# Kernel optimization log

Hardware: AMD Instinct MI355X
Metric: run time of the kernel (lower is better)

## Reference

```python
import jax, jax.numpy as jnp
import numpy as np

B, L, NSTATE = 8192, 256, 9


def setup_inputs() -> dict:
    key = jax.random.key(0)
    k1, k2, k3, k4 = jax.random.split(key, 4)
    inputs = jax.random.normal(k1, (B, L, NSTATE), dtype=jnp.float32)
    path = jax.random.randint(k2, (B, L), 0, NSTATE, dtype=jnp.int32)
    # learned CRF params (init'd to zeros in the module; use small random for a
    # non-degenerate reference)
    tran = jax.random.normal(k3, (NSTATE, NSTATE), dtype=jnp.float32) * 0.1
    init = jax.random.normal(k4, (NSTATE,), dtype=jnp.float32) * 0.1
    return {"inputs": inputs, "path": path, "tran": tran, "init": init}


def reference(inputs, path, tran, init):
    # inputs: [B, L, S], path: [B, L], tran: [S, S], init: [S]
    # bio=False -> mask and imask are all zeros (no-op additions).
    # --- gold path score ---
    emit = jnp.take_along_axis(inputs, path[..., None], axis=-1)[..., 0]  # [B, L]
    tran_sc = tran[path[..., :-1], path[..., 1:]]                         # [B, L-1]
    path_scores = emit.sum(-1) + init[path[..., 0]] + tran_sc.sum(-1)     # [B]

    # --- partition function via log-semiring forward recurrence ---
    alpha0 = init + inputs[..., 0, :]                                     # [B, S]

    def step(alpha, x_t):
        # alpha: [B, S] (prev state), x_t: [B, S] (emission at t)
        nxt = alpha[..., :, None] + tran + x_t[..., None, :]              # [B, S, S]
        return jax.nn.logsumexp(nxt, axis=-2), None

    xs = jnp.moveaxis(inputs[..., 1:, :], -2, 0)                          # [L-1, B, S]
    alpha, _ = jax.lax.scan(step, alpha0, xs)
    scores = jax.nn.logsumexp(alpha, axis=-1)                             # [B]
    return scores - path_scores
```

## Files before the change

### kernel.cpp

```cpp
#include <hip/hip_runtime.h>


#define B_N 8192
#define L_N 256
#define SEQ_STRIDE 2304
#define HALF 128
#define SPB 6
#define XW 54
#define XSTRIDE 55
#define NBLK 22
#define PLS 129
#define SPW 16
#define NDIR_BLOCKS (B_N / SPW)

#define LOG2E 1.44269504088896340736f
#define LN2f  0.69314718055994530942f

#define QP1 57
#define QP2 78
#define QP3 147
#define QROT(src, CTRL) \
  __int_as_float(__builtin_amdgcn_mov_dpp(__float_as_int(src), CTRL, 0xf, 0xf, 0))

#define WAITV0 asm volatile("s_waitcnt vmcnt(0)" ::: "memory")

__device__ __forceinline__ void gl_lds4(const void* g, void* l) {
  __builtin_amdgcn_global_load_lds(
      (const __attribute__((address_space(1))) void*)g,
      (__attribute__((address_space(3))) void*)l, 4, 0, 0);
}

__device__ __forceinline__ float fexp(float x) {
  return __builtin_amdgcn_exp2f(x * LOG2E);
}

#define FWD_STEP_BODY(KK, DO_RESC)                                          \
  do {                                                                      \
    float g[4][3];                                                          \
    _Pragma("unroll") for (int k = 0; k < 3; ++k) {                         \
      g[0][k] = o[k];                                                       \
      g[1][k] = QROT(o[k], QP1);                                            \
      g[2][k] = QROT(o[k], QP2);                                            \
      g[3][k] = QROT(o[k], QP3);                                            \
    }                                                                       \
    if (DO_RESC) {                                                          \
      float m = g[0][0];                                                    \
      _Pragma("unroll") for (int r = 0; r < 4; ++r)                         \
        _Pragma("unroll") for (int k = 0; k < 3; ++k)                       \
          m = fmaxf(m, g[r][k]);                                            \
      const int ex = (int)((__float_as_uint(m) >> 23) & 0xffu) - 126;       \
      ce += ex;                                                             \
      const float sc = __uint_as_float((unsigned)(127 - ex) << 23);         \
      _Pragma("unroll") for (int r = 0; r < 4; ++r)                         \
        _Pragma("unroll") for (int k = 0; k < 3; ++k)                       \
          g[r][k] *= sc;                                                    \
    }                                                                       \
    float out3[3];                                                          \
    _Pragma("unroll") for (int i = 0; i < 3; ++i) {                         \
      float a = Erot[0][0][i] * g[0][0];                                    \
      _Pragma("unroll") for (int r = 0; r < 4; ++r)                         \
        _Pragma("unroll") for (int k = 0; k < 3; ++k)                       \
          if (r + k > 0) a = fmaf(Erot[r][k][i], g[r][k], a);               \
      out3[i] = a;                                                          \
    }                                                                       \
    _Pragma("unroll") for (int i = 0; i < 3; ++i)                           \
      o[i] = out3[i] * e[(KK) * 3 + i];                                     \
  } while (0)

#define BWD_STEP_BODY(KK, DO_RESC)                                          \
  do {                                                                      \
    const int tt_ = 5 - (KK);                                               \
    float wv[3];                                                            \
    _Pragma("unroll") for (int k = 0; k < 3; ++k)                           \
      wv[k] = e[tt_ * 3 + k] * o[k];                                        \
    float g[4][3];                                                          \
    _Pragma("unroll") for (int k = 0; k < 3; ++k) {                         \
      g[0][k] = wv[k];                                                      \
      g[1][k] = QROT(wv[k], QP1);                                           \
      g[2][k] = QROT(wv[k], QP2);                                           \
      g[3][k] = QROT(wv[k], QP3);                                           \
    }                                                                       \
    if (DO_RESC) {                                                          \
      float m = g[0][0];                                                    \
      _Pragma("unroll") for (int r = 0; r < 4; ++r)                         \
        _Pragma("unroll") for (int k = 0; k < 3; ++k)                       \
          m = fmaxf(m, g[r][k]);                                            \
      const int ex = (int)((__float_as_uint(m) >> 23) & 0xffu) - 126;       \
      ce += ex;                                                             \
      const float sc = __uint_as_float((unsigned)(127 - ex) << 23);         \
      _Pragma("unroll") for (int r = 0; r < 4; ++r)                         \
        _Pragma("unroll") for (int k = 0; k < 3; ++k)                       \
          g[r][k] *= sc;                                                    \
    }                                                                       \
    float out3[3];                                                          \
    _Pragma("unroll") for (int i = 0; i < 3; ++i) {                         \
      float a = Erot[0][0][i] * g[0][0];                                    \
      _Pragma("unroll") for (int r = 0; r < 4; ++r)                         \
        _Pragma("unroll") for (int k = 0; k < 3; ++k)                       \
          if (r + k > 0) a = fmaf(Erot[r][k][i], g[r][k], a);               \
      out3[i] = a;                                                          \
    }                                                                       \
    _Pragma("unroll") for (int i = 0; i < 3; ++i) o[i] = out3[i];           \
  } while (0)

#define PREFETCH_WIN(NB)                                                    \
  if (lane < XW) {                                                          \
    const int fb = fwd ? (NB) * XW : (SEQ_STRIDE - XW * ((NB) + 1));        \
    float* dst = &lx[(NB) & 1][0];                                          \
    _Pragma("unroll") for (int r = 0; r < SPW; ++r)                         \
      gl_lds4(xg + (size_t)(seq0 + r) * SEQ_STRIDE + fb + lane,             \
              dst + r * XSTRIDE);                                           \
  }

#define EBATCH(T0, T1)                                                      \
  _Pragma("unroll") for (int tt = (T0); tt <= (T1); ++tt)                   \
    _Pragma("unroll") for (int k = 0; k < 3; ++k)                           \
      e[tt * 3 + k] = fexp(lxq[tt * 9 + myoff + k]);

#define EMTR_FWD(N)                                                         \
  _Pragma("unroll") for (int kk = 0; kk < (N); ++kk) {                      \
    em[kk] = lxq[kk * 9 + pc6[kk]];                                         \
    const int pp = kk ? pc6[kk - 1] : pcur;                                 \
    tr[kk] = ltran[pp * 9 + pc6[kk]];                                       \
  }

#define EMTR_BWD(N)                                                         \
  _Pragma("unroll") for (int kk = 0; kk < (N); ++kk) {                      \
    const int pc = kk ? pc6[kk - 1] : pcur;                                 \
    em[kk] = lxq[(5 - kk) * 9 + pc];                                        \
    tr[kk] = ltran[pc6[kk] * 9 + pc];                                       \
  }

#define PREREAD_PN(TBN)                                                     \
  if (fwd) {                                                                \
    _Pragma("unroll") for (int kk = 0; kk < SPB; ++kk) {                    \
      int t = (TBN) + kk; if (t > HALF - 1) t = HALF - 1;                   \
      pn6[kk] = plr[t];                                                     \
    }                                                                       \
  } else {                                                                  \
    _Pragma("unroll") for (int kk = 0; kk < SPB; ++kk) {                    \
      int idx = 127 - (TBN) - kk; if (idx < 0) idx = 0;                     \
      pn6[kk] = plr[idx];                                                   \
    }                                                                       \
  }

__global__ __launch_bounds__(64, 1) void crf_half(
    const float* __restrict__ xg, const int* __restrict__ path,
    const float* __restrict__ tran, const float* __restrict__ initv,
    float* __restrict__ ws)
{
  __shared__ float lx[2][SPW * XSTRIDE];
  __shared__ int   pl[SPW * PLS];
  __shared__ int   pl255[SPW];
  __shared__ float ltran[81];

  const int lane = threadIdx.x;
  const int c = lane & 3;
  const int q = lane >> 2;
  const bool fwd = (int)blockIdx.x < NDIR_BLOCKS;
  const int seq0 = (fwd ? blockIdx.x : blockIdx.x - NDIR_BLOCKS) * SPW;

  for (int i = lane; i < 81; i += 64) ltran[i] = tran[i];

  {
    const int t0 = fwd ? 0 : 127;
#pragma unroll
    for (int r = 0; r < SPW; ++r) {
      const int* g = path + (size_t)(seq0 + r) * L_N + t0 + lane;
      gl_lds4(g,      &pl[r * PLS]);
      gl_lds4(g + 64, &pl[r * PLS + 64]);
    }
  }
  if (!fwd && lane < SPW)
    pl255[lane] = path[(size_t)(seq0 + lane) * L_N + 255];
  if (lane < XW) {
    const int fb = fwd ? 0 : (SEQ_STRIDE - XW);
#pragma unroll
    for (int r = 0; r < SPW; ++r)
      gl_lds4(xg + (size_t)(seq0 + r) * SEQ_STRIDE + fb + lane,
              &lx[0][r * XSTRIDE]);
  }

  float Erot[4][3][3];
#pragma unroll
  for (int r = 0; r < 4; ++r)
#pragma unroll
    for (int k = 0; k < 3; ++k)
#pragma unroll
      for (int i = 0; i < 3; ++i) {
        const int ig = 3 * c + i;
        const int jg = 3 * ((c + r) & 3) + k;
        float v = 0.f;
        if (ig < 9 && jg < 9)
          v = fexp(fwd ? tran[jg * 9 + ig] : tran[ig * 9 + jg]);
        Erot[r][k][i] = v;
      }

  float iv[3];
#pragma unroll
  for (int k = 0; k < 3; ++k) {
    iv[k] = (fwd && c < 3) ? initv[3 * c + k] : 0.f;
    asm volatile("" :: "v"(iv[k]));
  }

  float o[3];
  float emit = 0.f, trn = 0.f;
  int ce = 0, pcur = 0;
  if (!fwd) {
#pragma unroll
    for (int k = 0; k < 3; ++k) o[k] = (c < 3) ? 1.f : 0.f;
  }

  const int myoff = (c == 3) ? 0 : 3 * c;
  const int* plr = &pl[q * PLS];

  WAITV0;
  if (!fwd) pcur = pl255[q];

  int pc6[SPB];
  if (fwd) {
#pragma unroll
    for (int kk = 0; kk < SPB; ++kk) pc6[kk] = plr[kk];
  } else {
#pragma unroll
    for (int kk = 0; kk < SPB; ++kk) pc6[kk] = plr[127 - kk];
  }

  {
    PREFETCH_WIN(1)
    const float* lxq = &lx[0][q * XSTRIDE];
    float e[SPB * 3];
    EBATCH(0, 5)
    float em[SPB], tr[SPB];
    int pn6[SPB];
    if (fwd) { EMTR_FWD(6) } else { EMTR_BWD(6) }
    PREREAD_PN(SPB)
    if (fwd) {
#pragma unroll
      for (int k = 0; k < 3; ++k)
        o[k] = (c < 3) ? fexp(iv[k] + lxq[myoff + k]) : 0.f;
      FWD_STEP_BODY(1, false);
      FWD_STEP_BODY(2, false);
      FWD_STEP_BODY(3, false);
      FWD_STEP_BODY(4, false);
      FWD_STEP_BODY(5, false);
#pragma unroll
      for (int kk = 0; kk < 6; ++kk) emit += em[kk];
#pragma unroll
      for (int kk = 1; kk < 6; ++kk) trn += tr[kk];
    } else {
      BWD_STEP_BODY(0, false);
      BWD_STEP_BODY(1, false);
      BWD_STEP_BODY(2, false);
      BWD_STEP_BODY(3, false);
      BWD_STEP_BODY(4, false);
      BWD_STEP_BODY(5, false);
#pragma unroll
      for (int kk = 0; kk < 6; ++kk) { emit += em[kk]; trn += tr[kk]; }
    }
    pcur = pc6[SPB - 1];
#pragma unroll
    for (int kk = 0; kk < SPB; ++kk) pc6[kk] = pn6[kk];
  }

#pragma unroll 1
  for (int b = 1; b <= 20; ++b) {
    const int tb = b * SPB;
    WAITV0;
    PREFETCH_WIN(b + 1)
    const float* lxq = &lx[b & 1][q * XSTRIDE];
    float e[SPB * 3];
    EBATCH(0, 5)
    float em[SPB], tr[SPB];
    int pn6[SPB];
    if (fwd) { EMTR_FWD(6) } else { EMTR_BWD(6) }
    PREREAD_PN(tb + SPB)
    if (fwd) {
      FWD_STEP_BODY(0, true);
      FWD_STEP_BODY(1, false);
      FWD_STEP_BODY(2, false);
      FWD_STEP_BODY(3, false);
      FWD_STEP_BODY(4, false);
      FWD_STEP_BODY(5, false);
    } else {
      BWD_STEP_BODY(0, true);
      BWD_STEP_BODY(1, false);
      BWD_STEP_BODY(2, false);
      BWD_STEP_BODY(3, false);
      BWD_STEP_BODY(4, false);
      BWD_STEP_BODY(5, false);
    }
#pragma unroll
    for (int kk = 0; kk < 6; ++kk) { emit += em[kk]; trn += tr[kk]; }
    pcur = pc6[SPB - 1];
#pragma unroll
    for (int kk = 0; kk < SPB; ++kk) pc6[kk] = pn6[kk];
  }

  {
    WAITV0;
    const float* lxq = &lx[1][q * XSTRIDE];
    float e[SPB * 3];
    float em[SPB], tr[SPB];
    if (fwd) {
      EBATCH(0, 1)
      EMTR_FWD(2)
      FWD_STEP_BODY(0, true);
      FWD_STEP_BODY(1, false);
    } else {
      EBATCH(4, 5)
      EMTR_BWD(2)
      BWD_STEP_BODY(0, true);
      BWD_STEP_BODY(1, false);
    }
#pragma unroll
    for (int kk = 0; kk < 2; ++kk) { emit += em[kk]; trn += tr[kk]; }
  }

  const int sq = seq0 + q;
  float* wp = ws + sq;
  if (fwd) {
    if (c < 3) {
#pragma unroll
      for (int k = 0; k < 3; ++k) wp[(3 * c + k) * B_N] = o[k];
    } else {
      wp[9 * B_N] = (float)ce;
      wp[10 * B_N] = emit + trn + initv[plr[0]];
    }
  } else {
    if (c < 3) {
#pragma unroll
      for (int k = 0; k < 3; ++k) wp[(11 + 3 * c + k) * B_N] = o[k];
    } else {
      wp[20 * B_N] = (float)ce;
      wp[21 * B_N] = emit + trn;
    }
  }
}

__global__ __launch_bounds__(256) void crf_combine(
    const float* __restrict__ ws, float* __restrict__ out)
{
  const int s = blockIdx.x * 256 + threadIdx.x;
  float dot = 0.f;
#pragma unroll
  for (int i = 0; i < 9; ++i)
    dot = fmaf(ws[i * B_N + s], ws[(11 + i) * B_N + s], dot);
  const float score =
      (__builtin_amdgcn_logf(dot) + ws[9 * B_N + s] + ws[20 * B_N + s]) * LN2f;
  out[s] = score - (ws[10 * B_N + s] + ws[21 * B_N + s]);
}

extern "C" void kernel_launch(void* const* d_in, const int* in_sizes, int n_in,
                              void* d_out, int out_size, void* d_ws, size_t ws_size,
                              hipStream_t stream) {
  (void)in_sizes; (void)n_in; (void)out_size; (void)ws_size;
  const float* xg    = (const float*)d_in[0];
  const int*   path  = (const int*)d_in[1];
  const float* tran  = (const float*)d_in[2];
  const float* initv = (const float*)d_in[3];
  float* ws  = (float*)d_ws;
  float* out = (float*)d_out;

  crf_half<<<2 * NDIR_BLOCKS, 64, 0, stream>>>(xg, path, tran, initv, ws);
  crf_combine<<<B_N / 256, 256, 0, stream>>>(ws, out);
}
```

Before: 126.5 us.

## Triple-buffer emission windows and software-pipeline exp/gather one block ahead

```diff
diff --git a/kernel.cpp b/kernel.cpp
--- a/kernel.cpp
+++ b/kernel.cpp
@@ -8,7 +8,6 @@
 #define SPB 6
 #define XW 54
 #define XSTRIDE 55
-#define NBLK 22
 #define PLS 129
 #define SPW 16
 #define NDIR_BLOCKS (B_N / SPW)
@@ -22,7 +21,8 @@
 #define QROT(src, CTRL) \
   __int_as_float(__builtin_amdgcn_mov_dpp(__float_as_int(src), CTRL, 0xf, 0xf, 0))
 
-#define WAITV0 asm volatile("s_waitcnt vmcnt(0)" ::: "memory")
+#define WAITV0  asm volatile("s_waitcnt vmcnt(0)" ::: "memory")
+#define WAITV16 asm volatile("s_waitcnt vmcnt(16)" ::: "memory")
 
 __device__ __forceinline__ void gl_lds4(const void* g, void* l) {
   __builtin_amdgcn_global_load_lds(
@@ -34,7 +34,7 @@
   return __builtin_amdgcn_exp2f(x * LOG2E);
 }
 
-#define FWD_STEP_BODY(KK, DO_RESC)                                          \
+#define FWD_STEP_BODY(KK, EA, DO_RESC)                                      \
   do {                                                                      \
     float g[4][3];                                                          \
     _Pragma("unroll") for (int k = 0; k < 3; ++k) {                         \
@@ -64,15 +64,15 @@
       out3[i] = a;                                                          \
     }                                                                       \
     _Pragma("unroll") for (int i = 0; i < 3; ++i)                           \
-      o[i] = out3[i] * e[(KK) * 3 + i];                                     \
+      o[i] = out3[i] * EA[(KK) * 3 + i];                                    \
   } while (0)
 
-#define BWD_STEP_BODY(KK, DO_RESC)                                          \
+#define BWD_STEP_BODY(KK, EA, DO_RESC)                                      \
   do {                                                                      \
     const int tt_ = 5 - (KK);                                               \
     float wv[3];                                                            \
     _Pragma("unroll") for (int k = 0; k < 3; ++k)                           \
-      wv[k] = e[tt_ * 3 + k] * o[k];                                        \
+      wv[k] = EA[tt_ * 3 + k] * o[k];                                       \
     float g[4][3];                                                          \
     _Pragma("unroll") for (int k = 0; k < 3; ++k) {                         \
       g[0][k] = wv[k];                                                      \
@@ -106,42 +106,48 @@
 #define PREFETCH_WIN(NB)                                                    \
   if (lane < XW) {                                                          \
     const int fb = fwd ? (NB) * XW : (SEQ_STRIDE - XW * ((NB) + 1));        \
-    float* dst = &lx[(NB) & 1][0];                                          \
+    float* dst = &lx[(NB) % 3][0];                                          \
     _Pragma("unroll") for (int r = 0; r < SPW; ++r)                         \
       gl_lds4(xg + (size_t)(seq0 + r) * SEQ_STRIDE + fb + lane,             \
               dst + r * XSTRIDE);                                           \
   }
 
-#define EBATCH(T0, T1)                                                      \
-  _Pragma("unroll") for (int tt = (T0); tt <= (T1); ++tt)                   \
+#define EBATCH_TO(EA, LXQ)                                                  \
+  _Pragma("unroll") for (int tt = 0; tt < 6; ++tt)                          \
     _Pragma("unroll") for (int k = 0; k < 3; ++k)                           \
-      e[tt * 3 + k] = fexp(lxq[tt * 9 + myoff + k]);
-
-#define EMTR_FWD(N)                                                         \
-  _Pragma("unroll") for (int kk = 0; kk < (N); ++kk) {                      \
-    em[kk] = lxq[kk * 9 + pc6[kk]];                                         \
-    const int pp = kk ? pc6[kk - 1] : pcur;                                 \
-    tr[kk] = ltran[pp * 9 + pc6[kk]];                                       \
-  }
-
-#define EMTR_BWD(N)                                                         \
-  _Pragma("unroll") for (int kk = 0; kk < (N); ++kk) {                      \
-    const int pc = kk ? pc6[kk - 1] : pcur;                                 \
-    em[kk] = lxq[(5 - kk) * 9 + pc];                                        \
-    tr[kk] = ltran[pc6[kk] * 9 + pc];                                       \
-  }
-
-#define PREREAD_PN(TBN)                                                     \
+      EA[tt * 3 + k] = fexp((LXQ)[tt * 9 + myoff + k]);
+
+#define EMTR_FWD_TO(EMA, TRA, LXQ, PCA, PPREV)                              \
+  _Pragma("unroll") for (int kk = 0; kk < 6; ++kk) {                        \
+    EMA[kk] = (LXQ)[kk * 9 + PCA[kk]];                                      \
+    const int pp_ = kk ? PCA[kk - 1] : (PPREV);                             \
+    TRA[kk] = ltran[pp_ * 9 + PCA[kk]];                                     \
+  }
+
+#define EMTR_BWD_TO(EMA, TRA, LXQ, PCA, PPREV)                              \
+  _Pragma("unroll") for (int kk = 0; kk < 6; ++kk) {                        \
+    const int pc_ = kk ? PCA[kk - 1] : (PPREV);                             \
+    EMA[kk] = (LXQ)[(5 - kk) * 9 + pc_];                                    \
+    TRA[kk] = ltran[PCA[kk] * 9 + pc_];                                     \
+  }
+
+#define PREREAD_TO(PNA, TBN)                                                \
   if (fwd) {                                                                \
-    _Pragma("unroll") for (int kk = 0; kk < SPB; ++kk) {                    \
-      int t = (TBN) + kk; if (t > HALF - 1) t = HALF - 1;                   \
-      pn6[kk] = plr[t];                                                     \
+    _Pragma("unroll") for (int kk = 0; kk < 6; ++kk) {                      \
+      int t_ = (TBN) + kk; if (t_ > HALF - 1) t_ = HALF - 1;                \
+      PNA[kk] = plr[t_];                                                    \
     }                                                                       \
   } else {                                                                  \
-    _Pragma("unroll") for (int kk = 0; kk < SPB; ++kk) {                    \
-      int idx = 127 - (TBN) - kk; if (idx < 0) idx = 0;                     \
-      pn6[kk] = plr[idx];                                                   \
-    }                                                                       \
+    _Pragma("unroll") for (int kk = 0; kk < 6; ++kk) {                      \
+      int idx_ = 127 - (TBN) - kk; if (idx_ < 0) idx_ = 0;                  \
+      PNA[kk] = plr[idx_];                                                  \
+    }                                                                       \
+  }
+
+#define ROTATE_NEXT                                                         \
+  _Pragma("unroll") for (int j = 0; j < 18; ++j) eC[j] = eN[j];             \
+  _Pragma("unroll") for (int j = 0; j < 6; ++j) {                           \
+    emC[j] = emN[j]; trC[j] = trN[j]; pcC[j] = pcN[j]; pcN[j] = pnN[j];     \
   }
 
 __global__ __launch_bounds__(64, 1) void crf_half(
@@ -149,7 +155,7 @@
     const float* __restrict__ tran, const float* __restrict__ initv,
     float* __restrict__ ws)
 {
-  __shared__ float lx[2][SPW * XSTRIDE];
+  __shared__ float lx[3][SPW * XSTRIDE];
   __shared__ int   pl[SPW * PLS];
   __shared__ int   pl255[SPW];
   __shared__ float ltran[81];
@@ -161,6 +167,8 @@
   const int seq0 = (fwd ? blockIdx.x : blockIdx.x - NDIR_BLOCKS) * SPW;
 
   for (int i = lane; i < 81; i += 64) ltran[i] = tran[i];
+  if (!fwd && lane < SPW)
+    pl255[lane] = path[(size_t)(seq0 + lane) * L_N + 255];
 
   {
     const int t0 = fwd ? 0 : 127;
@@ -171,14 +179,15 @@
       gl_lds4(g + 64, &pl[r * PLS + 64]);
     }
   }
-  if (!fwd && lane < SPW)
-    pl255[lane] = path[(size_t)(seq0 + lane) * L_N + 255];
   if (lane < XW) {
-    const int fb = fwd ? 0 : (SEQ_STRIDE - XW);
-#pragma unroll
-    for (int r = 0; r < SPW; ++r)
-      gl_lds4(xg + (size_t)(seq0 + r) * SEQ_STRIDE + fb + lane,
-              &lx[0][r * XSTRIDE]);
+#pragma unroll
+    for (int wi = 0; wi < 2; ++wi) {
+      const int fb = fwd ? wi * XW : (SEQ_STRIDE - XW * (wi + 1));
+#pragma unroll
+      for (int r = 0; r < SPW; ++r)
+        gl_lds4(xg + (size_t)(seq0 + r) * SEQ_STRIDE + fb + lane,
+                &lx[wi][r * XSTRIDE]);
+    }
   }
 
   float Erot[4][3][3];
@@ -217,104 +226,105 @@
   WAITV0;
   if (!fwd) pcur = pl255[q];
 
-  int pc6[SPB];
+  int pcC[6], pcN[6];
   if (fwd) {
 #pragma unroll
-    for (int kk = 0; kk < SPB; ++kk) pc6[kk] = plr[kk];
+    for (int kk = 0; kk < 6; ++kk) pcC[kk] = plr[kk];
   } else {
 #pragma unroll
-    for (int kk = 0; kk < SPB; ++kk) pc6[kk] = plr[127 - kk];
-  }
-
+    for (int kk = 0; kk < 6; ++kk) pcC[kk] = plr[127 - kk];
+  }
+  float eC[18], emC[6], trC[6];
   {
-    PREFETCH_WIN(1)
-    const float* lxq = &lx[0][q * XSTRIDE];
-    float e[SPB * 3];
-    EBATCH(0, 5)
-    float em[SPB], tr[SPB];
-    int pn6[SPB];
-    if (fwd) { EMTR_FWD(6) } else { EMTR_BWD(6) }
-    PREREAD_PN(SPB)
+    const float* lxq0 = &lx[0][q * XSTRIDE];
+    EBATCH_TO(eC, lxq0)
+    if (fwd) { EMTR_FWD_TO(emC, trC, lxq0, pcC, pcur) }
+    else     { EMTR_BWD_TO(emC, trC, lxq0, pcC, pcur) }
+  }
+  float xv0[3];
+#pragma unroll
+  for (int k = 0; k < 3; ++k) xv0[k] = lx[0][q * XSTRIDE + myoff + k];
+  PREREAD_TO(pcN, SPB)
+
+  {
+    PREFETCH_WIN(2)
+    WAITV16;
+    const float* lxqN = &lx[1][q * XSTRIDE];
+    float eN[18], emN[6], trN[6]; int pnN[6];
+    EBATCH_TO(eN, lxqN)
+    if (fwd) { EMTR_FWD_TO(emN, trN, lxqN, pcN, pcC[5]) }
+    else     { EMTR_BWD_TO(emN, trN, lxqN, pcN, pcC[5]) }
+    PREREAD_TO(pnN, 2 * SPB)
     if (fwd) {
 #pragma unroll
       for (int k = 0; k < 3; ++k)
-        o[k] = (c < 3) ? fexp(iv[k] + lxq[myoff + k]) : 0.f;
-      FWD_STEP_BODY(1, false);
-      FWD_STEP_BODY(2, false);
-      FWD_STEP_BODY(3, false);
-      FWD_STEP_BODY(4, false);
-      FWD_STEP_BODY(5, false);
-#pragma unroll
-      for (int kk = 0; kk < 6; ++kk) emit += em[kk];
-#pragma unroll
-      for (int kk = 1; kk < 6; ++kk) trn += tr[kk];
-    } else {
-      BWD_STEP_BODY(0, false);
-      BWD_STEP_BODY(1, false);
-      BWD_STEP_BODY(2, false);
-      BWD_STEP_BODY(3, false);
-      BWD_STEP_BODY(4, false);
-      BWD_STEP_BODY(5, false);
-#pragma unroll
-      for (int kk = 0; kk < 6; ++kk) { emit += em[kk]; trn += tr[kk]; }
-    }
-    pcur = pc6[SPB - 1];
-#pragma unroll
-    for (int kk = 0; kk < SPB; ++kk) pc6[kk] = pn6[kk];
+        o[k] = (c < 3) ? fexp(iv[k] + xv0[k]) : 0.f;
+      FWD_STEP_BODY(1, eC, false);
+      FWD_STEP_BODY(2, eC, false);
+      FWD_STEP_BODY(3, eC, false);
+      FWD_STEP_BODY(4, eC, false);
+      FWD_STEP_BODY(5, eC, false);
+#pragma unroll
+      for (int kk = 0; kk < 6; ++kk) emit += emC[kk];
+#pragma unroll
+      for (int kk = 1; kk < 6; ++kk) trn += trC[kk];
+    } else {
+      BWD_STEP_BODY(0, eC, false);
+      BWD_STEP_BODY(1, eC, false);
+      BWD_STEP_BODY(2, eC, false);
+      BWD_STEP_BODY(3, eC, false);
+      BWD_STEP_BODY(4, eC, false);
+      BWD_STEP_BODY(5, eC, false);
+#pragma unroll
+      for (int kk = 0; kk < 6; ++kk) { emit += emC[kk]; trn += trC[kk]; }
+    }
+    ROTATE_NEXT
   }
 
 #pragma unroll 1
   for (int b = 1; b <= 20; ++b) {
-    const int tb = b * SPB;
-    WAITV0;
-    PREFETCH_WIN(b + 1)
-    const float* lxq = &lx[b & 1][q * XSTRIDE];
-    float e[SPB * 3];
-    EBATCH(0, 5)
-    float em[SPB], tr[SPB];
-    int pn6[SPB];
-    if (fwd) { EMTR_FWD(6) } else { EMTR_BWD(6) }
-    PREREAD_PN(tb + SPB)
+    if (b + 2 <= 21) {
+      PREFETCH_WIN(b + 2)
+      WAITV16;
+    } else {
+      WAITV0;
+    }
+    const float* lxqN = &lx[(b + 1) % 3][q * XSTRIDE];
+    float eN[18], emN[6], trN[6]; int pnN[6];
+    EBATCH_TO(eN, lxqN)
+    if (fwd) { EMTR_FWD_TO(emN, trN, lxqN, pcN, pcC[5]) }
+    else     { EMTR_BWD_TO(emN, trN, lxqN, pcN, pcC[5]) }
+    PREREAD_TO(pnN, (b + 2) * SPB)
     if (fwd) {
-      FWD_STEP_BODY(0, true);
-      FWD_STEP_BODY(1, false);
-      FWD_STEP_BODY(2, false);
-      FWD_STEP_BODY(3, false);
-      FWD_STEP_BODY(4, false);
-      FWD_STEP_BODY(5, false);
-    } else {
-      BWD_STEP_BODY(0, true);
-      BWD_STEP_BODY(1, false);
-      BWD_STEP_BODY(2, false);
-      BWD_STEP_BODY(3, false);
-      BWD_STEP_BODY(4, false);
-      BWD_STEP_BODY(5, false);
-    }
-#pragma unroll
-    for (int kk = 0; kk < 6; ++kk) { emit += em[kk]; trn += tr[kk]; }
-    pcur = pc6[SPB - 1];
-#pragma unroll
-    for (int kk = 0; kk < SPB; ++kk) pc6[kk] = pn6[kk];
+      FWD_STEP_BODY(0, eC, true);
+      FWD_STEP_BODY(1, eC, false);
+      FWD_STEP_BODY(2, eC, false);
+      FWD_STEP_BODY(3, eC, false);
+      FWD_STEP_BODY(4, eC, false);
+      FWD_STEP_BODY(5, eC, false);
+    } else {
+      BWD_STEP_BODY(0, eC, true);
+      BWD_STEP_BODY(1, eC, false);
+      BWD_STEP_BODY(2, eC, false);
+      BWD_STEP_BODY(3, eC, false);
+      BWD_STEP_BODY(4, eC, false);
+      BWD_STEP_BODY(5, eC, false);
+    }
+#pragma unroll
+    for (int kk = 0; kk < 6; ++kk) { emit += emC[kk]; trn += trC[kk]; }
+    ROTATE_NEXT
   }
 
   {
-    WAITV0;
-    const float* lxq = &lx[1][q * XSTRIDE];
-    float e[SPB * 3];
-    float em[SPB], tr[SPB];
     if (fwd) {
-      EBATCH(0, 1)
-      EMTR_FWD(2)
-      FWD_STEP_BODY(0, true);
-      FWD_STEP_BODY(1, false);
-    } else {
-      EBATCH(4, 5)
-      EMTR_BWD(2)
-      BWD_STEP_BODY(0, true);
-      BWD_STEP_BODY(1, false);
-    }
-#pragma unroll
-    for (int kk = 0; kk < 2; ++kk) { emit += em[kk]; trn += tr[kk]; }
+      FWD_STEP_BODY(0, eC, true);
+      FWD_STEP_BODY(1, eC, false);
+    } else {
+      BWD_STEP_BODY(0, eC, true);
+      BWD_STEP_BODY(1, eC, false);
+    }
+#pragma unroll
+    for (int kk = 0; kk < 2; ++kk) { emit += emC[kk]; trn += trC[kk]; }
   }
 
   const int sq = seq0 + q;
```

Result: no change. 126.9 us (+0.3%).
